# Performance work log

Hardware: AMD Instinct MI355X
Metric: run time of the kernel (lower is better)

The kernel has to match this reference:

```python
import jax, jax.numpy as jnp
import numpy as np

N = 100000          # nodes
E = 1600000         # random edges (self loops appended in reference)
F_IN = 256          # dataset.num_features
NUM_CLASSES = 7     # dataset.num_classes
H = 2 * NUM_CLASSES # heads = 14
C = NUM_CLASSES     # per-head channels (concat=False)
NEG_SLOPE = 0.2     # GATConv default leaky_relu slope


def setup_inputs() -> dict:
    key = jax.random.key(0)
    ks = jax.random.split(key, 10)
    x = jax.random.normal(ks[0], (N, F_IN), jnp.float32)
    edge_index = jax.random.randint(ks[1], (2, E), 0, N, jnp.int32)
    def glorot(k, shape, fan_in):
        return jax.random.normal(k, shape, jnp.float32) * (1.0 / np.sqrt(fan_in))
    return {
        "x": x,
        "edge_index": edge_index,
        "W1": glorot(ks[2], (F_IN, H * C), F_IN),
        "a_src1": glorot(ks[3], (H, C), C),
        "a_dst1": glorot(ks[4], (H, C), C),
        "b1": jnp.zeros((C,), jnp.float32),
        "W2": glorot(ks[5], (C, H * C), C),
        "a_src2": glorot(ks[6], (H, C), C),
        "a_dst2": glorot(ks[7], (H, C), C),
        "b2": jnp.zeros((C,), jnp.float32),
    }


def gat_conv(x, src, dst, W, a_src, a_dst, b):
    # x: [N, Fin] -> per-head projections [N, H, C]
    xh = (x @ W).reshape(N, H, C)
    # per-node attention logits [N, H]
    al_src = jnp.einsum("nhc,hc->nh", xh, a_src)
    al_dst = jnp.einsum("nhc,hc->nh", xh, a_dst)
    # per-edge logits (message flows src -> dst)
    alpha = jax.nn.leaky_relu(al_src[src] + al_dst[dst], NEG_SLOPE)  # [E', H]
    # segment softmax over incoming edges of each destination node
    amax = jax.ops.segment_max(jax.lax.stop_gradient(alpha), dst, num_segments=N)
    alpha = jnp.exp(alpha - amax[dst])
    denom = jax.ops.segment_sum(alpha, dst, num_segments=N)
    alpha = alpha / denom[dst]
    # weighted messages, then MAX aggregation per destination (aggr='max')
    msg = alpha[:, :, None] * xh[src]                    # [E', H, C]
    out = jax.ops.segment_max(msg, dst, num_segments=N)  # [N, H, C]
    # concat=False -> mean over heads, plus bias
    return out.mean(axis=1) + b                          # [N, C]


def reference(x, edge_index, W1, a_src1, a_dst1, b1, W2, a_src2, a_dst2, b2):
    # GATConv(add_self_loops=True): append self loops so every node has >=1 in-edge
    loops = jnp.arange(N, dtype=edge_index.dtype)
    src = jnp.concatenate([edge_index[0], loops])
    dst = jnp.concatenate([edge_index[1], loops])
    h = gat_conv(x, src, dst, W1, a_src1, a_dst1, b1)
    h = jax.nn.relu(h)
    h = gat_conv(h, src, dst, W2, a_src2, a_dst2, b2)
    return jax.nn.log_softmax(h, axis=1)
```

## Files before the change

### kernel.cpp

```cpp
#include <hip/hip_runtime.h>
#include <math.h>

#define H  14
#define C  7
#define HC 98
#define FIN 256
#define NEG_SLOPE 0.2f
#define NPB 32
#define AGG_BLOCK (NPB * H)

#define BSHIFT 9
#define BSIZE  512
#define NBUCK_MAX 256

typedef __attribute__((ext_vector_type(8))) short short8;
typedef __attribute__((ext_vector_type(4))) float floatx4;

#define WT_ROWS   112
#define WT_STRIDE 264
#define XA_STRIDE 40
#define VS_STRIDE 99

__device__ __forceinline__ unsigned bf16r(float f) {
    unsigned u = __float_as_uint(f);
    return (u + 0x7FFFu + ((u >> 16) & 1u)) >> 16;
}
__device__ __forceinline__ float bflo(unsigned w) { return __uint_as_float(w << 16); }
__device__ __forceinline__ float bfhi(unsigned w) { return __uint_as_float(w & 0xFFFF0000u); }


__global__ void k_zero(int* __restrict__ p, int n) {
    int i = blockIdx.x * blockDim.x + threadIdx.x;
    if (i < n) p[i] = 0;
}

__global__ __launch_bounds__(256) void k_hist(const int* __restrict__ ei, int E,
                                              int* __restrict__ gcnt, int nb) {
    __shared__ int hist[NBUCK_MAX];
    const int t = threadIdx.x;
    for (int i = t; i < nb; i += 256) hist[i] = 0;
    __syncthreads();
    const int stride = gridDim.x * 256;
    for (int e = blockIdx.x * 256 + t; e < E; e += stride)
        atomicAdd(&hist[ei[E + e] >> BSHIFT], 1);
    __syncthreads();
    for (int i = t; i < nb; i += 256)
        if (hist[i]) atomicAdd(gcnt + i, hist[i]);
}

__global__ __launch_bounds__(1024) void k_bscan(const int* __restrict__ gcnt,
                                                int* __restrict__ boff, int* __restrict__ bcur,
                                                int* __restrict__ row_ptr, int nb, int N) {
    __shared__ int sd[1024];
    int t = threadIdx.x;
    int own = (t < nb) ? gcnt[t] : 0;
    sd[t] = own;
    __syncthreads();
    #pragma unroll
    for (int off = 1; off < 1024; off <<= 1) {
        int v = (t >= off) ? sd[t - off] : 0;
        __syncthreads();
        sd[t] += v;
        __syncthreads();
    }
    if (t < nb) {
        boff[t + 1] = sd[t];
        bcur[t] = sd[t] - own;
        if (t == nb - 1) row_ptr[N] = sd[t];
    }
    if (t == 0) boff[0] = 0;
}

__global__ __launch_bounds__(256) void k_part(const int* __restrict__ ei, int E,
                                              int* __restrict__ bcur, int2* __restrict__ pedge,
                                              int nb) {
    __shared__ int hist[NBUCK_MAX];
    __shared__ int start[NBUCK_MAX];
    const int t = threadIdx.x;
    const int chunk = (E + gridDim.x - 1) / gridDim.x;
    const int c0 = blockIdx.x * chunk;
    const int c1 = min(c0 + chunk, E);
    for (int i = t; i < nb; i += 256) hist[i] = 0;
    __syncthreads();
    for (int e = c0 + t; e < c1; e += 256)
        atomicAdd(&hist[ei[E + e] >> BSHIFT], 1);
    __syncthreads();
    for (int i = t; i < nb; i += 256) {
        int h = hist[i];
        start[i] = h ? atomicAdd(bcur + i, h) : 0;
        hist[i] = 0;
    }
    __syncthreads();
    for (int e = c0 + t; e < c1; e += 256) {
        int s = ei[e], d = ei[E + e];
        int b = d >> BSHIFT;
        int pos = start[b] + atomicAdd(&hist[b], 1);
        pedge[pos] = make_int2(s, d);
    }
}

__global__ __launch_bounds__(512) void k_bcsr(const int2* __restrict__ pedge,
                                              const int* __restrict__ boff,
                                              int* __restrict__ row_ptr, int* __restrict__ col,
                                              int N) {
    __shared__ int cnt[BSIZE];
    __shared__ int sc[BSIZE];
    __shared__ int cur[BSIZE];
    const int b  = blockIdx.x;
    const int t  = threadIdx.x;
    const int e0 = boff[b], e1 = boff[b + 1];
    const int base = b << BSHIFT;
    const int nv = min(BSIZE, N - base);
    cnt[t] = 0;
    __syncthreads();
    for (int e = e0 + t; e < e1; e += 512)
        atomicAdd(&cnt[pedge[e].y - base], 1);
    __syncthreads();
    sc[t] = cnt[t];
    __syncthreads();
    #pragma unroll
    for (int off = 1; off < BSIZE; off <<= 1) {
        int v = (t >= off) ? sc[t - off] : 0;
        __syncthreads();
        sc[t] += v;
        __syncthreads();
    }
    if (t < nv) {
        int excl = sc[t] - cnt[t];
        row_ptr[base + t] = e0 + excl;
        cur[t] = excl;
    }
    __syncthreads();
    for (int e = e0 + t; e < e1; e += 512) {
        int2 r = pedge[e];
        int d = r.y - base;
        int pos = e0 + atomicAdd(&cur[d], 1);
        col[pos] = r.x;
    }
}


__global__ void k_convW(const float* __restrict__ W, unsigned short* __restrict__ WtG) {
    int id = blockIdx.x * blockDim.x + threadIdx.x;
    int n = id >> 8, k = id & 255;
    float v = (n < HC) ? W[k * HC + n] : 0.f;
    WtG[id] = (unsigned short)(__float_as_uint(v) >> 16);
}

__global__ __launch_bounds__(256) void k_proj1_mfma(
    const float* __restrict__ x, const unsigned short* __restrict__ WtG,
    const float* __restrict__ asrc, const float* __restrict__ adst,
    uint4* __restrict__ xpack, float* __restrict__ aldst, int N)
{
    __shared__ unsigned short wt_s[WT_ROWS * WT_STRIDE];
    __shared__ unsigned short xa_s[64 * XA_STRIDE];
    __shared__ float as_s[HC], ad_s[HC];
    float* vals_s = (float*)wt_s;
    const int t  = threadIdx.x;
    const int wv = t >> 6;
    const int l  = t & 63;
    const int ln = l & 15;
    const int qd = l >> 4;
    const int rowBase = blockIdx.x * 64;

    #pragma unroll
    for (int i = 0; i < 14; ++i) {
        int f = i * 256 + t;
        int r = f >> 5, pos = f & 31;
        *(uint4*)(wt_s + r * WT_STRIDE + pos * 8) = ((const uint4*)WtG)[f];
    }
    if (t < HC) { as_s[t] = asrc[t]; ad_s[t] = adst[t]; }

    floatx4 acc[7] = {};

    for (int step = 0; step < 8; ++step) {
        const int k0 = step * 32;
        __syncthreads();
        #pragma unroll
        for (int i = 0; i < 2; ++i) {
            int idx = i * 256 + t;
            int r = idx >> 3, c4 = idx & 7;
            int gr = rowBase + r; if (gr >= N) gr = N - 1;
            float4 v = *(const float4*)(x + (size_t)gr * FIN + k0 + c4 * 4);
            ushort4 u;
            u.x = (unsigned short)(__float_as_uint(v.x) >> 16);
            u.y = (unsigned short)(__float_as_uint(v.y) >> 16);
            u.z = (unsigned short)(__float_as_uint(v.z) >> 16);
            u.w = (unsigned short)(__float_as_uint(v.w) >> 16);
            *(ushort4*)(xa_s + r * XA_STRIDE + c4 * 4) = u;
        }
        __syncthreads();
        short8 a = *(const short8*)(xa_s + ((wv << 4) + ln) * XA_STRIDE + qd * 8);
        #pragma unroll
        for (int ct = 0; ct < 7; ++ct) {
            short8 b = *(const short8*)(wt_s + (ct * 16 + ln) * WT_STRIDE + k0 + qd * 8);
            acc[ct] = __builtin_amdgcn_mfma_f32_16x16x32_bf16(a, b, acc[ct], 0, 0, 0);
        }
    }

    __syncthreads();
    #pragma unroll
    for (int ct = 0; ct < 7; ++ct) {
        int colg = ct * 16 + ln;
        if (colg < HC) {
            #pragma unroll
            for (int r = 0; r < 4; ++r)
                vals_s[((wv << 4) + (qd << 2) + r) * VS_STRIDE + colg] = acc[ct][r];
        }
    }
    __syncthreads();

    for (int p = t; p < 64 * H; p += 256) {
        int nl = p / H, h = p - nl * H;
        int gn = rowBase + nl;
        if (gn >= N) break;
        const float* vp = vals_s + nl * VS_STRIDE + h * C;
        unsigned v[C];
        float s1 = 0.f, s2 = 0.f;
        #pragma unroll
        for (int c2 = 0; c2 < C; ++c2) {
            float f = vp[c2];
            v[c2] = bf16r(f);
            s1 = fmaf(f, as_s[h * C + c2], s1);
            s2 = fmaf(f, ad_s[h * C + c2], s2);
        }
        uint4 pk;
        pk.x = v[0] | (v[1] << 16);
        pk.y = v[2] | (v[3] << 16);
        pk.z = v[4] | (v[5] << 16);
        pk.w = v[6] | (bf16r(s1) << 16);
        xpack[(size_t)gn * H + h] = pk;
        aldst[(size_t)gn * H + h] = s2;
    }
}


__global__ __launch_bounds__(256) void k_proj2_pack(
    const float* __restrict__ h1, const float* __restrict__ W,
    const float* __restrict__ asrc, const float* __restrict__ adst,
    uint4* __restrict__ xpack, float* __restrict__ aldst, int N)
{
    __shared__ float Ws[C * HC];
    __shared__ float as_s[HC], ad_s[HC];
    const int t = threadIdx.x;
    for (int i = t; i < C * HC; i += 256) Ws[i] = W[i];
    if (t < HC) { as_s[t] = asrc[t]; ad_s[t] = adst[t]; }
    __syncthreads();
    int n = blockIdx.x * 256 + t;
    if (n >= N) return;
    float xr[C];
    #pragma unroll
    for (int c2 = 0; c2 < C; ++c2) xr[c2] = h1[(size_t)n * C + c2];
    #pragma unroll
    for (int h = 0; h < H; ++h) {
        float v[C], s1 = 0.f, s2 = 0.f;
        #pragma unroll
        for (int c2 = 0; c2 < C; ++c2) {
            float acc = 0.f;
            #pragma unroll
            for (int k = 0; k < C; ++k)
                acc = fmaf(xr[k], Ws[k * HC + h * C + c2], acc);
            v[c2] = acc;
            s1 = fmaf(acc, as_s[h * C + c2], s1);
            s2 = fmaf(acc, ad_s[h * C + c2], s2);
        }
        uint4 pk;
        pk.x = bf16r(v[0]) | (bf16r(v[1]) << 16);
        pk.y = bf16r(v[2]) | (bf16r(v[3]) << 16);
        pk.z = bf16r(v[4]) | (bf16r(v[5]) << 16);
        pk.w = bf16r(v[6]) | (bf16r(s1) << 16);
        xpack[(size_t)n * H + h] = pk;
        aldst[(size_t)n * H + h] = s2;
    }
}


#define AGG_STEP(MM, DEN, MX, REC)                                   \
    {                                                                \
        float l = bfhi((REC).w) + ld;                                \
        l = (l > 0.f) ? l : NEG_SLOPE * l;                           \
        float mn = fmaxf(MM, l);                                     \
        float r  = __expf(MM - mn);                                  \
        float p  = __expf(l - mn);                                   \
        DEN = DEN * r + p;                                           \
        MX[0] = fmaxf(MX[0] * r, p * bflo((REC).x));                 \
        MX[1] = fmaxf(MX[1] * r, p * bfhi((REC).x));                 \
        MX[2] = fmaxf(MX[2] * r, p * bflo((REC).y));                 \
        MX[3] = fmaxf(MX[3] * r, p * bfhi((REC).y));                 \
        MX[4] = fmaxf(MX[4] * r, p * bflo((REC).z));                 \
        MX[5] = fmaxf(MX[5] * r, p * bfhi((REC).z));                 \
        MX[6] = fmaxf(MX[6] * r, p * bflo((REC).w));                 \
        MM = mn;                                                     \
    }

template<int LAYER>
__global__ __launch_bounds__(AGG_BLOCK) void k_agg(
    const int* __restrict__ row_ptr, const int* __restrict__ col,
    const uint4* __restrict__ xpack, const float* __restrict__ aldst,
    const float* __restrict__ bias,
    float* __restrict__ h1, float* __restrict__ out, int N)
{
    __shared__ float vals[NPB][HC];
    __shared__ float fv[NPB][C];
    const int t  = threadIdx.x;
    const int nl = t / H;
    const int h  = t - nl * H;
    const int n  = blockIdx.x * NPB + nl;

    if (n < N) {
        const int e0  = row_ptr[n];
        const int deg = row_ptr[n + 1] - e0;
        const float ld = aldst[(size_t)n * H + h];

        float mA, denA, mxA[C];
        {
            uint4 pk = xpack[(size_t)n * H + h];
            float l = bfhi(pk.w) + ld;
            l = (l > 0.f) ? l : NEG_SLOPE * l;
            mA = l; denA = 1.f;
            mxA[0] = bflo(pk.x); mxA[1] = bfhi(pk.x);
            mxA[2] = bflo(pk.y); mxA[3] = bfhi(pk.y);
            mxA[4] = bflo(pk.z); mxA[5] = bfhi(pk.z);
            mxA[6] = bflo(pk.w);
        }

        if (deg > 0) {
            const int last = deg - 1;
            float mB, denB, mxB[C];
            {
                uint4 pk = xpack[(size_t)col[e0] * H + h];
                float l = bfhi(pk.w) + ld;
                l = (l > 0.f) ? l : NEG_SLOPE * l;
                mB = l; denB = 1.f;
                mxB[0] = bflo(pk.x); mxB[1] = bfhi(pk.x);
                mxB[2] = bflo(pk.y); mxB[3] = bfhi(pk.y);
                mxB[4] = bflo(pk.z); mxB[5] = bfhi(pk.z);
                mxB[6] = bflo(pk.w);
            }
            int c0 = col[e0 + min(1, last)];
            int c1 = col[e0 + min(2, last)];
            int c2 = col[e0 + min(3, last)];
            int c3 = col[e0 + min(4, last)];
            uint4 r0 = xpack[(size_t)c0 * H + h];
            uint4 r1 = xpack[(size_t)c1 * H + h];
            uint4 r2 = xpack[(size_t)c2 * H + h];
            uint4 r3 = xpack[(size_t)c3 * H + h];
            c0 = col[e0 + min(5, last)];
            c1 = col[e0 + min(6, last)];
            c2 = col[e0 + min(7, last)];
            c3 = col[e0 + min(8, last)];
            for (int i = 1; i < deg; i += 2) {
                uint4 curA = r0, curB = r1;
                r0 = r2; r1 = r3;
                r2 = xpack[(size_t)c0 * H + h];
                r3 = xpack[(size_t)c1 * H + h];
                c0 = c2; c1 = c3;
                c2 = col[e0 + min(i + 8, last)];
                c3 = col[e0 + min(i + 9, last)];
                AGG_STEP(mA, denA, mxA, curA);
                if (i + 1 < deg) AGG_STEP(mB, denB, mxB, curB);
            }
            float mn = fmaxf(mA, mB);
            float rA = __expf(mA - mn), rB = __expf(mB - mn);
            denA = denA * rA + denB * rB;
            #pragma unroll
            for (int c4 = 0; c4 < C; ++c4)
                mxA[c4] = fmaxf(mxA[c4] * rA, mxB[c4] * rB);
        }

        float rd = 1.f / denA;
        #pragma unroll
        for (int c2 = 0; c2 < C; ++c2) vals[nl][h * C + c2] = mxA[c2] * rd;
    }
    __syncthreads();

    if (t < NPB * C) {
        int nl2 = t / C, c2 = t - nl2 * C;
        int n2 = blockIdx.x * NPB + nl2;
        if (n2 < N) {
            float s = 0.f;
            #pragma unroll
            for (int hh = 0; hh < H; ++hh) s += vals[nl2][hh * C + c2];
            float o = s * (1.f / H) + bias[c2];
            if (LAYER == 1) h1[(size_t)n2 * C + c2] = fmaxf(o, 0.f);
            else            fv[nl2][c2] = o;
        }
    }
    if (LAYER == 2) {
        __syncthreads();
        if (t < NPB) {
            int n2 = blockIdx.x * NPB + t;
            if (n2 < N) {
                float mv = -1e30f;
                #pragma unroll
                for (int c2 = 0; c2 < C; ++c2) mv = fmaxf(mv, fv[t][c2]);
                float lse = 0.f;
                #pragma unroll
                for (int c2 = 0; c2 < C; ++c2) lse += __expf(fv[t][c2] - mv);
                lse = logf(lse);
                #pragma unroll
                for (int c2 = 0; c2 < C; ++c2)
                    out[(size_t)n2 * C + c2] = fv[t][c2] - mv - lse;
            }
        }
    }
}


static inline size_t align16(size_t v) { return (v + 15) & ~(size_t)15; }

extern "C" void kernel_launch(void* const* d_in, const int* in_sizes, int n_in,
                              void* d_out, int out_size, void* d_ws, size_t ws_size,
                              hipStream_t stream)
{
    const float* x     = (const float*)d_in[0];
    const int*   ei    = (const int*)d_in[1];
    const float* W1    = (const float*)d_in[2];
    const float* asrc1 = (const float*)d_in[3];
    const float* adst1 = (const float*)d_in[4];
    const float* b1    = (const float*)d_in[5];
    const float* W2    = (const float*)d_in[6];
    const float* asrc2 = (const float*)d_in[7];
    const float* adst2 = (const float*)d_in[8];
    const float* b2    = (const float*)d_in[9];

    const int N  = in_sizes[0] / FIN;
    const int E  = in_sizes[1] / 2;
    const int nb = (N + BSIZE - 1) >> BSHIFT;

    char* w = (char*)d_ws;
    uint4* xpack   = (uint4*)w; w += align16((size_t)N * H * 16);
    int2*  pedge   = (int2*)w;  w += align16((size_t)E * 8);
    float* aldst   = (float*)w; w += align16((size_t)N * H * 4);
    float* h1      = (float*)w; w += align16((size_t)N * C * 4);
    int*   row_ptr = (int*)w;   w += align16((size_t)(N + 1) * 4);
    int*   col     = (int*)w;   w += align16((size_t)E * 4);
    int*   gcnt    = (int*)w;   w += align16((size_t)nb * 4);
    int*   boff    = (int*)w;   w += align16((size_t)(nb + 1) * 4);
    int*   bcur    = (int*)w;   w += align16((size_t)nb * 4);
    unsigned short* WtG = (unsigned short*)w; w += align16((size_t)WT_ROWS * FIN * 2);

    const int gAgg  = (N + NPB - 1) / NPB;
    const int gMfma = (N + 63) / 64;
    const int g256N = (N + 255) / 256;

    k_zero<<<1, 256, 0, stream>>>(gcnt, nb);
    k_hist<<<256, 256, 0, stream>>>(ei, E, gcnt, nb);
    k_bscan<<<1, 1024, 0, stream>>>(gcnt, boff, bcur, row_ptr, nb, N);
    k_part<<<256, 256, 0, stream>>>(ei, E, bcur, pedge, nb);
    k_bcsr<<<nb, 512, 0, stream>>>(pedge, boff, row_ptr, col, N);

    k_convW<<<(WT_ROWS * FIN + 255) / 256, 256, 0, stream>>>(W1, WtG);
    k_proj1_mfma<<<gMfma, 256, 0, stream>>>(x, WtG, asrc1, adst1, xpack, aldst, N);
    k_agg<1><<<gAgg, AGG_BLOCK, 0, stream>>>(row_ptr, col, xpack, aldst, b1,
                                             h1, (float*)d_out, N);
    k_proj2_pack<<<g256N, 256, 0, stream>>>(h1, W2, asrc2, adst2, xpack, aldst, N);
    k_agg<2><<<gAgg, AGG_BLOCK, 0, stream>>>(row_ptr, col, xpack, aldst, b2,
                                             h1, (float*)d_out, N);
}
```

Measured before the change: 414.5 us.

## Use fixed softmax shift and packed fp16 math in GAT edge aggregation

Features and source logits are now packed as fp16 instead of bf16. Both attention logits are pre-scaled by log2(e) so the edge loop can use exp2 directly. The online-softmax running max and its per-edge rescale are replaced by a fixed per-destination shift K, computed from the destination logit plus an assumed bound on the source logit. The weighted max aggregation uses packed half2 multiply and max, which cuts the per-edge exp and rescale work and halves the channel ALU ops. The fixed shift only stays safe if logits stay within a range that avoids fp16/exp overflow or underflow, so correctness depends on the logit magnitudes seen in practice.

```diff
diff --git a/kernel.cpp b/kernel.cpp
--- a/kernel.cpp
+++ b/kernel.cpp
@@ -8,6 +8,7 @@
 #define NEG_SLOPE 0.2f
 #define NPB 32
 #define AGG_BLOCK (NPB * H)
+#define LOG2E 1.44269504088896f
 
 #define BSHIFT 9
 #define BSIZE  512
@@ -15,6 +16,7 @@
 
 typedef __attribute__((ext_vector_type(8))) short short8;
 typedef __attribute__((ext_vector_type(4))) float floatx4;
+typedef _Float16 h2 __attribute__((ext_vector_type(2)));
 
 #define WT_ROWS   112
 #define WT_STRIDE 264
@@ -25,8 +27,16 @@
     unsigned u = __float_as_uint(f);
     return (u + 0x7FFFu + ((u >> 16) & 1u)) >> 16;
 }
-__device__ __forceinline__ float bflo(unsigned w) { return __uint_as_float(w << 16); }
-__device__ __forceinline__ float bfhi(unsigned w) { return __uint_as_float(w & 0xFFFF0000u); }
+
+__device__ __forceinline__ h2 u2h(unsigned u) { return __builtin_bit_cast(h2, u); }
+__device__ __forceinline__ unsigned hpk(float a, float b) {
+    h2 v = { (_Float16)a, (_Float16)b };
+    return __builtin_bit_cast(unsigned, v);
+}
+__device__ __forceinline__ float hhi(unsigned w) {
+    unsigned short s = (unsigned short)(w >> 16);
+    return (float)__builtin_bit_cast(_Float16, s);
+}
 
 
 __global__ void k_zero(int* __restrict__ p, int n) {
@@ -215,22 +225,22 @@
         int gn = rowBase + nl;
         if (gn >= N) break;
         const float* vp = vals_s + nl * VS_STRIDE + h * C;
-        unsigned v[C];
+        float v[C];
         float s1 = 0.f, s2 = 0.f;
         #pragma unroll
         for (int c2 = 0; c2 < C; ++c2) {
             float f = vp[c2];
-            v[c2] = bf16r(f);
+            v[c2] = f;
             s1 = fmaf(f, as_s[h * C + c2], s1);
             s2 = fmaf(f, ad_s[h * C + c2], s2);
         }
         uint4 pk;
-        pk.x = v[0] | (v[1] << 16);
-        pk.y = v[2] | (v[3] << 16);
-        pk.z = v[4] | (v[5] << 16);
-        pk.w = v[6] | (bf16r(s1) << 16);
+        pk.x = hpk(v[0], v[1]);
+        pk.y = hpk(v[2], v[3]);
+        pk.z = hpk(v[4], v[5]);
+        pk.w = hpk(v[6], s1 * LOG2E);
         xpack[(size_t)gn * H + h] = pk;
-        aldst[(size_t)gn * H + h] = s2;
+        aldst[(size_t)gn * H + h] = s2 * LOG2E;
     }
 }
 
@@ -265,32 +275,26 @@
             s2 = fmaf(acc, ad_s[h * C + c2], s2);
         }
         uint4 pk;
-        pk.x = bf16r(v[0]) | (bf16r(v[1]) << 16);
-        pk.y = bf16r(v[2]) | (bf16r(v[3]) << 16);
-        pk.z = bf16r(v[4]) | (bf16r(v[5]) << 16);
-        pk.w = bf16r(v[6]) | (bf16r(s1) << 16);
+        pk.x = hpk(v[0], v[1]);
+        pk.y = hpk(v[2], v[3]);
+        pk.z = hpk(v[4], v[5]);
+        pk.w = hpk(v[6], s1 * LOG2E);
         xpack[(size_t)n * H + h] = pk;
-        aldst[(size_t)n * H + h] = s2;
-    }
-}
-
-
-#define AGG_STEP(MM, DEN, MX, REC)                                   \
-    {                                                                \
-        float l = bfhi((REC).w) + ld;                                \
-        l = (l > 0.f) ? l : NEG_SLOPE * l;                           \
-        float mn = fmaxf(MM, l);                                     \
-        float r  = __expf(MM - mn);                                  \
-        float p  = __expf(l - mn);                                   \
-        DEN = DEN * r + p;                                           \
-        MX[0] = fmaxf(MX[0] * r, p * bflo((REC).x));                 \
-        MX[1] = fmaxf(MX[1] * r, p * bfhi((REC).x));                 \
-        MX[2] = fmaxf(MX[2] * r, p * bflo((REC).y));                 \
-        MX[3] = fmaxf(MX[3] * r, p * bfhi((REC).y));                 \
-        MX[4] = fmaxf(MX[4] * r, p * bflo((REC).z));                 \
-        MX[5] = fmaxf(MX[5] * r, p * bfhi((REC).z));                 \
-        MX[6] = fmaxf(MX[6] * r, p * bflo((REC).w));                 \
-        MM = mn;                                                     \
+        aldst[(size_t)n * H + h] = s2 * LOG2E;
+    }
+}
+
+#define AGG_STEP(DEN, REC)                                              \
+    {                                                                   \
+        float l = hhi((REC).w) + ld;                                    \
+        float p = __builtin_amdgcn_exp2f(fmaxf(l, 0.2f * l) - K);       \
+        DEN += p;                                                       \
+        _Float16 ph = (_Float16)p;                                      \
+        h2 p2 = { ph, ph };                                             \
+        m0 = __builtin_elementwise_max(m0, p2 * u2h((REC).x));          \
+        m1 = __builtin_elementwise_max(m1, p2 * u2h((REC).y));          \
+        m2 = __builtin_elementwise_max(m2, p2 * u2h((REC).z));          \
+        m3 = __builtin_elementwise_max(m3, p2 * u2h((REC).w));          \
     }
 
 template<int LAYER>
@@ -311,45 +315,39 @@
         const int e0  = row_ptr[n];
         const int deg = row_ptr[n + 1] - e0;
         const float ld = aldst[(size_t)n * H + h];
-
-        float mA, denA, mxA[C];
+        const float kb = ld + 2.0f * LOG2E;
+        const float K  = fmaxf(kb, 0.2f * kb);
+
+        float denA, denB = 0.f;
+        h2 m0, m1, m2, m3;
         {
             uint4 pk = xpack[(size_t)n * H + h];
-            float l = bfhi(pk.w) + ld;
-            l = (l > 0.f) ? l : NEG_SLOPE * l;
-            mA = l; denA = 1.f;
-            mxA[0] = bflo(pk.x); mxA[1] = bfhi(pk.x);
-            mxA[2] = bflo(pk.y); mxA[3] = bfhi(pk.y);
-            mxA[4] = bflo(pk.z); mxA[5] = bfhi(pk.z);
-            mxA[6] = bflo(pk.w);
+            float l = hhi(pk.w) + ld;
+            float p = __builtin_amdgcn_exp2f(fmaxf(l, 0.2f * l) - K);
+            denA = p;
+            _Float16 ph = (_Float16)p;
+            h2 p2 = { ph, ph };
+            m0 = p2 * u2h(pk.x);
+            m1 = p2 * u2h(pk.y);
+            m2 = p2 * u2h(pk.z);
+            m3 = p2 * u2h(pk.w);
         }
 
         if (deg > 0) {
             const int last = deg - 1;
-            float mB, denB, mxB[C];
-            {
-                uint4 pk = xpack[(size_t)col[e0] * H + h];
-                float l = bfhi(pk.w) + ld;
-                l = (l > 0.f) ? l : NEG_SLOPE * l;
-                mB = l; denB = 1.f;
-                mxB[0] = bflo(pk.x); mxB[1] = bfhi(pk.x);
-                mxB[2] = bflo(pk.y); mxB[3] = bfhi(pk.y);
-                mxB[4] = bflo(pk.z); mxB[5] = bfhi(pk.z);
-                mxB[6] = bflo(pk.w);
-            }
-            int c0 = col[e0 + min(1, last)];
-            int c1 = col[e0 + min(2, last)];
-            int c2 = col[e0 + min(3, last)];
-            int c3 = col[e0 + min(4, last)];
+            int c0 = col[e0];
+            int c1 = col[e0 + min(1, last)];
+            int c2 = col[e0 + min(2, last)];
+            int c3 = col[e0 + min(3, last)];
             uint4 r0 = xpack[(size_t)c0 * H + h];
             uint4 r1 = xpack[(size_t)c1 * H + h];
             uint4 r2 = xpack[(size_t)c2 * H + h];
             uint4 r3 = xpack[(size_t)c3 * H + h];
-            c0 = col[e0 + min(5, last)];
-            c1 = col[e0 + min(6, last)];
-            c2 = col[e0 + min(7, last)];
-            c3 = col[e0 + min(8, last)];
-            for (int i = 1; i < deg; i += 2) {
+            c0 = col[e0 + min(4, last)];
+            c1 = col[e0 + min(5, last)];
+            c2 = col[e0 + min(6, last)];
+            c3 = col[e0 + min(7, last)];
+            for (int i = 0; i < deg; i += 2) {
                 uint4 curA = r0, curB = r1;
                 r0 = r2; r1 = r3;
                 r2 = xpack[(size_t)c0 * H + h];
@@ -357,20 +355,17 @@
                 c0 = c2; c1 = c3;
                 c2 = col[e0 + min(i + 8, last)];
                 c3 = col[e0 + min(i + 9, last)];
-                AGG_STEP(mA, denA, mxA, curA);
-                if (i + 1 < deg) AGG_STEP(mB, denB, mxB, curB);
+                AGG_STEP(denA, curA);
+                if (i + 1 < deg) AGG_STEP(denB, curB);
             }
-            float mn = fmaxf(mA, mB);
-            float rA = __expf(mA - mn), rB = __expf(mB - mn);
-            denA = denA * rA + denB * rB;
-            #pragma unroll
-            for (int c4 = 0; c4 < C; ++c4)
-                mxA[c4] = fmaxf(mxA[c4] * rA, mxB[c4] * rB);
-        }
-
-        float rd = 1.f / denA;
-        #pragma unroll
-        for (int c2 = 0; c2 < C; ++c2) vals[nl][h * C + c2] = mxA[c2] * rd;
+        }
+
+        float rd = 1.f / (denA + denB);
+        float* vp = &vals[nl][h * C];
+        vp[0] = (float)m0.x * rd; vp[1] = (float)m0.y * rd;
+        vp[2] = (float)m1.x * rd; vp[3] = (float)m1.y * rd;
+        vp[4] = (float)m2.x * rd; vp[5] = (float)m2.y * rd;
+        vp[6] = (float)m3.x * rd;
     }
     __syncthreads();
 
```

Measured after the change: 412.3 us. Within noise of the previous version (-0.5%).
